# Kernel optimization log

Hardware: AMD Instinct MI355X
Metric: run time of the kernel (lower is better)

## Reference

```python
import jax, jax.numpy as jnp
import numpy as np

B, C, H, W = 4, 512, 32, 32
NUM_HEADS, DIM_HEAD = 16, 32
DIM_ATTN = NUM_HEADS * DIM_HEAD  # 512
N = H * W


def setup_inputs() -> dict:
    key = jax.random.key(0)
    ks = jax.random.split(key, 6)
    s = 0.02
    return {
        "x": jax.random.normal(ks[0], (B, C, H, W), jnp.float32),
        "w_qkv": jax.random.normal(ks[1], (3 * DIM_ATTN, C), jnp.float32) * s,
        "b_qkv": jax.random.normal(ks[2], (3 * DIM_ATTN,), jnp.float32) * s,
        "w_proj": jax.random.normal(ks[3], (C, DIM_ATTN), jnp.float32) * s,
        "b_proj": jax.random.normal(ks[4], (C,), jnp.float32) * s,
        "shared_rel_pos": jax.random.normal(ks[5], (1, NUM_HEADS, N, N), jnp.float32) * s,
    }


def reference(x, w_qkv, b_qkv, w_proj, b_proj, shared_rel_pos):
    b, c, h, w = x.shape
    n = h * w
    scale = DIM_HEAD ** -0.5
    # 1x1 conv == per-pixel matmul over channels
    qkv = jnp.einsum('bchw,oc->bohw', x, w_qkv) + b_qkv[None, :, None, None]
    # [B, heads, 3*dh, N] -> chunk along dim 2 (matches torch .chunk(3, dim=2))
    qkv = qkv.reshape(b, NUM_HEADS, 3 * DIM_HEAD, n)
    q, k, v = jnp.split(qkv, 3, axis=2)          # each [B, heads, dh, N]
    attn = jnp.einsum('bhdi,bhdj->bhij', q, k) * scale  # q^T @ k
    attn = attn + shared_rel_pos
    attn = jax.nn.softmax(attn, axis=-1)
    out = jnp.einsum('bhdj,bhij->bhdi', v, attn)  # v @ attn^T, [B, heads, dh, N]
    out = out.reshape(b, NUM_HEADS * DIM_HEAD, h, w)
    out = jnp.einsum('bchw,oc->bohw', out, w_proj) + b_proj[None, :, None, None]
    return out
```

## Files before the change

kernel.cpp:

```cpp
#include <hip/hip_runtime.h>
#include <cstdint>
#include <cstddef>

#define BATCH 4
#define CIN   512
#define NPIX  1024
#define HEADS 16
#define DH    32
#define DATTN 512
#define O_QKV 1536

typedef unsigned short u16;
typedef __bf16 bf16x4 __attribute__((ext_vector_type(4)));
typedef __bf16 bf16x8 __attribute__((ext_vector_type(8)));
typedef float  f32x4  __attribute__((ext_vector_type(4)));

typedef const __attribute__((address_space(1))) void g1_t;
typedef __attribute__((address_space(3))) void l3_t;

#if defined(__has_builtin)
#if __has_builtin(__builtin_amdgcn_exp2f)
#define EXP2(x) __builtin_amdgcn_exp2f(x)
#endif
#endif
#ifndef EXP2
#define EXP2(x) __expf((x) * 0.6931471805599453f)
#endif

__device__ __forceinline__ u16 f2bf(float f) {
  unsigned u = __float_as_uint(f);
  u += 0x7fffu + ((u >> 16) & 1u);
  return (u16)(u >> 16);
}

__device__ __forceinline__ void gl_lds16(const void* gp, void* lp) {
  __builtin_amdgcn_global_load_lds((g1_t*)gp, (l3_t*)lp, 16, 0, 0);
}

__global__ __launch_bounds__(256) void prep_fused(const float* __restrict__ x,
                                                  const float* __restrict__ w1,
                                                  const float* __restrict__ w2,
                                                  u16* __restrict__ xt,
                                                  u16* __restrict__ o1,
                                                  u16* __restrict__ o2) {
  const int t = threadIdx.x;
  if (blockIdx.x < 512) {
    __shared__ float sT[64][65];
    const int q  = blockIdx.x;
    const int n0 = (q & 15) << 6;
    const int c0 = ((q >> 4) & 7) << 6;
    const int b  = q >> 7;
    const float* xb = x + ((size_t)b * CIN + c0) * NPIX + n0;
#pragma unroll
    for (int i = 0; i < 4; ++i) {
      int r   = i * 16 + (t >> 4);
      int col = (t & 15) << 2;
      float4 v = *reinterpret_cast<const float4*>(&xb[(size_t)r * NPIX + col]);
      sT[r][col + 0] = v.x; sT[r][col + 1] = v.y;
      sT[r][col + 2] = v.z; sT[r][col + 3] = v.w;
    }
    __syncthreads();
#pragma unroll
    for (int i = 0; i < 2; ++i) {
      int nl = t >> 2;
      int ch = (t & 3) + (i << 2);
      u16 tmp[8];
#pragma unroll
      for (int e = 0; e < 8; ++e) tmp[e] = f2bf(sT[(ch << 3) + e][nl]);
      *reinterpret_cast<uint4*>(&xt[((size_t)b * NPIX + n0 + nl) * CIN + c0 + (ch << 3)]) =
          *reinterpret_cast<uint4*>(tmp);
    }
  } else {
    const int idx = (blockIdx.x - 512) * 256 + t;
    const int n1 = (O_QKV * CIN) >> 2;
    float4 v = (idx < n1) ? reinterpret_cast<const float4*>(w1)[idx]
                          : reinterpret_cast<const float4*>(w2)[idx - n1];
    uint2 pk = make_uint2((unsigned)f2bf(v.x) | ((unsigned)f2bf(v.y) << 16),
                          (unsigned)f2bf(v.z) | ((unsigned)f2bf(v.w) << 16));
    if (idx < n1) reinterpret_cast<uint2*>(o1)[idx] = pk;
    else          reinterpret_cast<uint2*>(o2)[idx - n1] = pk;
  }
}

__global__ __launch_bounds__(256) void gemm_qkv_mfma(const u16* __restrict__ wq,
                                                     const u16* __restrict__ xt,
                                                     const float* __restrict__ bias,
                                                     u16* __restrict__ qt,
                                                     u16* __restrict__ kt,
                                                     u16* __restrict__ vt) {
  __shared__ __align__(16) u16 sA[96 * 64];
  __shared__ __align__(16) u16 sB[128 * 64];
  const int t  = threadIdx.x;
  const int w  = t >> 6, l = t & 63, g = l >> 4, ln = l & 15;
  const int n0 = blockIdx.x * 128;
  const int h  = blockIdx.y;
  const int b  = blockIdx.z;
  const int wm = w >> 1, wn = w & 1;

  const u16* wbase = wq + (size_t)h * 96 * CIN;
  const u16* xbase = xt + ((size_t)b * NPIX + n0) * CIN;

  f32x4 acc[3][4];
#pragma unroll
  for (int mi = 0; mi < 3; ++mi)
#pragma unroll
    for (int ni = 0; ni < 4; ++ni) acc[mi][ni] = {0.f, 0.f, 0.f, 0.f};

  for (int k0 = 0; k0 < CIN; k0 += 64) {
#pragma unroll
    for (int i = 0; i < 3; ++i) {
      int chunk = i * 256 + (w << 6) + l;
      gl_lds16(wbase + ((size_t)(chunk >> 3)) * CIN + k0 + ((chunk & 7) << 3),
               (char*)sA + i * 4096 + (w << 10));
    }
#pragma unroll
    for (int i = 0; i < 4; ++i) {
      int chunk = i * 256 + (w << 6) + l;
      gl_lds16(xbase + ((size_t)(chunk >> 3)) * CIN + k0 + ((chunk & 7) << 3),
               (char*)sB + i * 4096 + (w << 10));
    }
    __syncthreads();
#pragma unroll
    for (int kk = 0; kk < 64; kk += 32) {
      bf16x8 af[3], bfr[4];
#pragma unroll
      for (int mi = 0; mi < 3; ++mi)
        af[mi] = *reinterpret_cast<const bf16x8*>(&sA[(48 * wm + 16 * mi + ln) * 64 + kk + (g << 3)]);
#pragma unroll
      for (int ni = 0; ni < 4; ++ni)
        bfr[ni] = *reinterpret_cast<const bf16x8*>(&sB[((wn << 6) + (ni << 4) + ln) * 64 + kk + (g << 3)]);
#pragma unroll
      for (int mi = 0; mi < 3; ++mi)
#pragma unroll
        for (int ni = 0; ni < 4; ++ni)
          acc[mi][ni] = __builtin_amdgcn_mfma_f32_16x16x32_bf16(af[mi], bfr[ni], acc[mi][ni], 0, 0, 0);
    }
    __syncthreads();
  }

  const float QSC = 0.17677669529663687f * 1.4426950408889634f;
  const float* bh = bias + h * 96;
#pragma unroll
  for (int mi = 0; mi < 3; ++mi) {
    const int sec = 48 * wm + 16 * mi;
    const int rb  = sec + (g << 2);
    const float b0 = bh[rb + 0], b1 = bh[rb + 1], b2 = bh[rb + 2], b3 = bh[rb + 3];
#pragma unroll
    for (int ni = 0; ni < 4; ++ni) {
      const int n = n0 + (wn << 6) + (ni << 4) + ln;
      f32x4 a = acc[mi][ni];
      float v0 = a[0] + b0, v1 = a[1] + b1, v2 = a[2] + b2, v3 = a[3] + b3;
      if (sec < 32) { v0 *= QSC; v1 *= QSC; v2 *= QSC; v3 *= QSC; }
      u16 e0 = f2bf(v0), e1 = f2bf(v1), e2 = f2bf(v2), e3 = f2bf(v3);
      if (sec < 32) {
        const int d = sec + (g << 2);
        uint2 pk = make_uint2((unsigned)e0 | ((unsigned)e1 << 16),
                              (unsigned)e2 | ((unsigned)e3 << 16));
        *reinterpret_cast<uint2*>(&qt[(((size_t)(b * HEADS + h)) * NPIX + n) * DH + d]) = pk;
      } else if (sec < 64) {
        const int d = sec - 32 + (g << 2);
        uint2 pk = make_uint2((unsigned)e0 | ((unsigned)e1 << 16),
                              (unsigned)e2 | ((unsigned)e3 << 16));
        *reinterpret_cast<uint2*>(&kt[(((size_t)(b * HEADS + h)) * NPIX + n) * DH + d]) = pk;
      } else {
        const int d = sec - 64 + (g << 2);
        u16* vp = &vt[(((size_t)(b * HEADS + h)) * DH + d) * NPIX + n];
        vp[0] = e0; vp[NPIX] = e1; vp[2 * NPIX] = e2; vp[3 * NPIX] = e3;
      }
    }
  }
}

__global__ __launch_bounds__(256, 2) void attn_mfma(const u16* __restrict__ qt,
                                                    const u16* __restrict__ kt,
                                                    const u16* __restrict__ vt,
                                                    const float* __restrict__ rel,
                                                    u16* __restrict__ aout) {
  __shared__ __align__(16) u16 sK[2][2][2048];
  __shared__ __align__(16) u16 sV[2][2][2048];
  __shared__ __align__(16) u16 sP[4][1024];

  const int t  = threadIdx.x;
  const int w  = t >> 6, l = t & 63, g = l >> 4, ln = l & 15;
  const int bid = blockIdx.x;
  const int xcd = bid & 7, sl = bid >> 3;
  const int bp  = sl & 1;
  const int i0  = ((sl >> 1) & 15) << 6;
  const int h   = (xcd << 1) | (sl >> 5);
  const int iw  = w;

  const size_t bh0 = (size_t)((bp * 2 + 0) * HEADS + h);
  const size_t bh1 = (size_t)((bp * 2 + 1) * HEADS + h);

  const int sc_r  = t >> 3;
  const int sc_kc = (t & 7) ^ (sc_r & 7) ^ ((sc_r >> 3) & 1);
  const int sc_vc = (t & 7) ^ (sc_r & 7);
  const size_t kro = ((size_t)((sc_r << 1) | (sc_kc >> 2))) * DH + ((sc_kc & 3) << 3);
  const u16* ksrc0 = kt + bh0 * NPIX * DH + kro;
  const u16* ksrc1 = kt + bh1 * NPIX * DH + kro;
  const u16* vsrc0 = vt + (bh0 * DH + sc_r) * NPIX + (sc_vc << 3);
  const u16* vsrc1 = vt + (bh1 * DH + sc_r) * NPIX + (sc_vc << 3);
  char* kBase = (char*)&sK[0][0][0] + (w << 10);
  char* vBase = (char*)&sV[0][0][0] + (w << 10);

#define STAGE(s_, p_) do {                                               \
    gl_lds16(ksrc0 + (size_t)(s_) * 2048, kBase + (p_) * 8192);          \
    gl_lds16(ksrc1 + (size_t)(s_) * 2048, kBase + (p_) * 8192 + 4096);   \
    gl_lds16(vsrc0 + (size_t)(s_) * 64,   vBase + (p_) * 8192);          \
    gl_lds16(vsrc1 + (size_t)(s_) * 64,   vBase + (p_) * 8192 + 4096);   \
  } while (0)

  STAGE(0, 0);

  bf16x8 qf0 = *reinterpret_cast<const bf16x8*>(
      qt + (bh0 * NPIX + i0 + (iw << 4) + ln) * DH + (g << 3));
  bf16x8 qf1 = *reinterpret_cast<const bf16x8*>(
      qt + (bh1 * NPIX + i0 + (iw << 4) + ln) * DH + (g << 3));

  const float* relp = rel + ((size_t)h * NPIX + i0 + (iw << 4) + (g << 2)) * NPIX +
                      (ln << 2);
  f32x4 relA4[4], relB4[4];
#pragma unroll
  for (int v = 0; v < 4; ++v)
    relA4[v] = *reinterpret_cast<const f32x4*>(relp + (size_t)v * NPIX);

  f32x4 vzero = {0.f, 0.f, 0.f, 0.f};
  f32x4 accO0[2] = {vzero, vzero};
  f32x4 accO1[2] = {vzero, vzero};
  f32x4 l_lane0 = vzero, l_lane1 = vzero;

  u16* sPw = &sP[w][0];
  const float LOG2E = 1.4426950408889634f;

  for (int s = 0; s < 16; ++s) {
    const int p = s & 1;
    __syncthreads();
    if (s < 15) {
      STAGE(s + 1, p ^ 1);
#pragma unroll
      for (int v = 0; v < 4; ++v)
        relB4[v] = *reinterpret_cast<const f32x4*>(relp + (size_t)v * NPIX + ((s + 1) << 6));
    }

#pragma unroll
    for (int b2 = 0; b2 < 2; ++b2) {
      const u16* Kb = &sK[p][b2][0];
      const u16* Vb = &sV[p][b2][0];
      const bf16x8 qf = b2 ? qf1 : qf0;

      f32x4 sfr[4];
      __builtin_amdgcn_s_setprio(1);
#pragma unroll
      for (int jj = 0; jj < 4; ++jj) {
        const int r  = (ln << 1) + (jj >> 1);
        const int ks = ((((jj & 1) << 2) | g) ^ (r & 7)) ^ ((r >> 3) & 1);
        bf16x8 kf = *reinterpret_cast<const bf16x8*>(Kb + r * 64 + ks * 8);
        sfr[jj] = __builtin_amdgcn_mfma_f32_16x16x32_bf16(qf, kf, vzero, 0, 0, 0);
      }
      __builtin_amdgcn_s_setprio(0);

#pragma unroll
      for (int v = 0; v < 4; ++v) {
        float p0 = EXP2(fmaf(relA4[v][0], LOG2E, sfr[0][v]));
        float p1 = EXP2(fmaf(relA4[v][1], LOG2E, sfr[1][v]));
        float p2 = EXP2(fmaf(relA4[v][2], LOG2E, sfr[2][v]));
        float p3 = EXP2(fmaf(relA4[v][3], LOG2E, sfr[3][v]));
        if (b2) l_lane1[v] += (p0 + p1) + (p2 + p3);
        else    l_lane0[v] += (p0 + p1) + (p2 + p3);
        bf16x4 pk;
        pk[0] = (__bf16)p0; pk[1] = (__bf16)p1; pk[2] = (__bf16)p2; pk[3] = (__bf16)p3;
        const int rw = (g << 2) + v;
        *reinterpret_cast<bf16x4*>(
            sPw + rw * 64 + ((((ln >> 1) ^ (rw & 7)) << 3) | ((ln & 1) << 2))) = pk;
      }

      __builtin_amdgcn_s_setprio(1);
#pragma unroll
      for (int kc = 0; kc < 2; ++kc) {
        const int lc = (kc << 2) | g;
        bf16x8 pa = *reinterpret_cast<const bf16x8*>(sPw + ln * 64 + ((lc ^ (ln & 7)) << 3));
#pragma unroll
        for (int dc = 0; dc < 2; ++dc) {
          const int d  = (dc << 4) + ln;
          const int vs = lc ^ (d & 7);
          bf16x8 vf = *reinterpret_cast<const bf16x8*>(Vb + d * 64 + vs * 8);
          if (b2) accO1[dc] = __builtin_amdgcn_mfma_f32_16x16x32_bf16(pa, vf, accO1[dc], 0, 0, 0);
          else    accO0[dc] = __builtin_amdgcn_mfma_f32_16x16x32_bf16(pa, vf, accO0[dc], 0, 0, 0);
        }
      }
      __builtin_amdgcn_s_setprio(0);
    }

    if (s < 15) {
#pragma unroll
      for (int v = 0; v < 4; ++v) relA4[v] = relB4[v];
    }
  }
#undef STAGE

#pragma unroll
  for (int v = 0; v < 4; ++v) {
    float ls = l_lane0[v];
    ls += __shfl_xor(ls, 1);
    ls += __shfl_xor(ls, 2);
    ls += __shfl_xor(ls, 4);
    ls += __shfl_xor(ls, 8);
    const float inv = 1.f / ls;
    const size_t row = (size_t)(bp * 2 + 0) * NPIX + i0 + (iw << 4) + (g << 2) + v;
    aout[row * DATTN + (h << 5) + ln]      = f2bf(accO0[0][v] * inv);
    aout[row * DATTN + (h << 5) + 16 + ln] = f2bf(accO0[1][v] * inv);
  }
#pragma unroll
  for (int v = 0; v < 4; ++v) {
    float ls = l_lane1[v];
    ls += __shfl_xor(ls, 1);
    ls += __shfl_xor(ls, 2);
    ls += __shfl_xor(ls, 4);
    ls += __shfl_xor(ls, 8);
    const float inv = 1.f / ls;
    const size_t row = (size_t)(bp * 2 + 1) * NPIX + i0 + (iw << 4) + (g << 2) + v;
    aout[row * DATTN + (h << 5) + ln]      = f2bf(accO1[0][v] * inv);
    aout[row * DATTN + (h << 5) + 16 + ln] = f2bf(accO1[1][v] * inv);
  }
}

__global__ __launch_bounds__(256) void gemm_proj_mfma(const u16* __restrict__ wp,
                                                      const u16* __restrict__ at,
                                                      const float* __restrict__ bias,
                                                      float* __restrict__ out) {
  __shared__ __align__(16) u16 sA[64 * 64];
  __shared__ __align__(16) u16 sB[128 * 64];
  const int t  = threadIdx.x;
  const int w  = t >> 6, l = t & 63, g = l >> 4, ln = l & 15;
  const int n0 = blockIdx.x * 128;
  const int o0 = blockIdx.y * 64;
  const int b  = blockIdx.z;
  const int wm = w >> 1, wn = w & 1;

  const u16* wbase = wp + (size_t)o0 * DATTN;
  const u16* abase = at + ((size_t)b * NPIX + n0) * DATTN;

  f32x4 acc[2][4];
#pragma unroll
  for (int mi = 0; mi < 2; ++mi)
#pragma unroll
    for (int ni = 0; ni < 4; ++ni) acc[mi][ni] = {0.f, 0.f, 0.f, 0.f};

  for (int k0 = 0; k0 < DATTN; k0 += 64) {
#pragma unroll
    for (int i = 0; i < 2; ++i) {
      int chunk = i * 256 + (w << 6) + l;
      gl_lds16(wbase + ((size_t)(chunk >> 3)) * DATTN + k0 + ((chunk & 7) << 3),
               (char*)sA + i * 4096 + (w << 10));
    }
#pragma unroll
    for (int i = 0; i < 4; ++i) {
      int chunk = i * 256 + (w << 6) + l;
      gl_lds16(abase + ((size_t)(chunk >> 3)) * DATTN + k0 + ((chunk & 7) << 3),
               (char*)sB + i * 4096 + (w << 10));
    }
    __syncthreads();
#pragma unroll
    for (int kk = 0; kk < 64; kk += 32) {
      bf16x8 af[2], bfr[4];
#pragma unroll
      for (int mi = 0; mi < 2; ++mi)
        af[mi] = *reinterpret_cast<const bf16x8*>(&sA[((wm << 5) + (mi << 4) + ln) * 64 + kk + (g << 3)]);
#pragma unroll
      for (int ni = 0; ni < 4; ++ni)
        bfr[ni] = *reinterpret_cast<const bf16x8*>(&sB[((wn << 6) + (ni << 4) + ln) * 64 + kk + (g << 3)]);
#pragma unroll
      for (int mi = 0; mi < 2; ++mi)
#pragma unroll
        for (int ni = 0; ni < 4; ++ni)
          acc[mi][ni] = __builtin_amdgcn_mfma_f32_16x16x32_bf16(af[mi], bfr[ni], acc[mi][ni], 0, 0, 0);
    }
    __syncthreads();
  }

#pragma unroll
  for (int mi = 0; mi < 2; ++mi) {
    const int o = o0 + (wm << 5) + (mi << 4) + (g << 2);
    const float b0 = bias[o], b1 = bias[o + 1], b2 = bias[o + 2], b3 = bias[o + 3];
#pragma unroll
    for (int ni = 0; ni < 4; ++ni) {
      const int n = n0 + (wn << 6) + (ni << 4) + ln;
      float* op = &out[((size_t)b * DATTN + o) * NPIX + n];
      op[0]        = acc[mi][ni][0] + b0;
      op[NPIX]     = acc[mi][ni][1] + b1;
      op[2 * NPIX] = acc[mi][ni][2] + b2;
      op[3 * NPIX] = acc[mi][ni][3] + b3;
    }
  }
}

extern "C" void kernel_launch(void* const* d_in, const int* in_sizes, int n_in,
                              void* d_out, int out_size, void* d_ws, size_t ws_size,
                              hipStream_t stream) {
  (void)in_sizes; (void)n_in; (void)out_size; (void)ws_size;
  const float* x      = (const float*)d_in[0];
  const float* w_qkv  = (const float*)d_in[1];
  const float* b_qkv  = (const float*)d_in[2];
  const float* w_proj = (const float*)d_in[3];
  const float* b_proj = (const float*)d_in[4];
  const float* rel    = (const float*)d_in[5];
  float* out = (float*)d_out;

  u16* xt    = (u16*)d_ws;
  u16* wq_bf = xt + (size_t)BATCH * NPIX * CIN;
  u16* wp_bf = wq_bf + (size_t)O_QKV * CIN;
  u16* qt    = wp_bf + (size_t)DATTN * DATTN;
  u16* kt    = qt + (size_t)BATCH * HEADS * NPIX * DH;
  u16* vt    = kt + (size_t)BATCH * HEADS * NPIX * DH;
  u16* aout  = vt + (size_t)BATCH * HEADS * NPIX * DH;

  prep_fused<<<1536, 256, 0, stream>>>(x, w_qkv, w_proj, xt, wq_bf, wp_bf);
  gemm_qkv_mfma<<<dim3(NPIX / 128, HEADS, BATCH), 256, 0, stream>>>(wq_bf, xt, b_qkv, qt, kt, vt);
  attn_mfma<<<512, 256, 0, stream>>>(qt, kt, vt, rel, aout);
  gemm_proj_mfma<<<dim3(NPIX / 128, DATTN / 64, BATCH), 256, 0, stream>>>(wp_bf, aout, b_proj, out);
}
```

Before: 62.74 us.

## Split attention key range across two wave groups and merge partial sums

The attention kernel now launches 512 threads per block. The upper four waves process the second half of the key/value sequence, and the lower four process the first half, so each wave runs half as many loop iterations. Partial output accumulators and row sums from the second half are passed through shared memory and added before normalisation. This needs no max rescaling, because the softmax has no max subtraction. The goal is more waves in flight and shorter per-wave latency on the key loop, at the cost of doubled LDS staging, an extra merge step with barriers, and a possible cap on occupancy from the larger shared memory footprint.

```diff
diff --git a/kernel.cpp b/kernel.cpp
--- a/kernel.cpp
+++ b/kernel.cpp
@@ -171,14 +171,14 @@
   }
 }
 
-__global__ __launch_bounds__(256, 2) void attn_mfma(const u16* __restrict__ qt,
+__global__ __launch_bounds__(512, 4) void attn_mfma(const u16* __restrict__ qt,
                                                     const u16* __restrict__ kt,
                                                     const u16* __restrict__ vt,
                                                     const float* __restrict__ rel,
                                                     u16* __restrict__ aout) {
-  __shared__ __align__(16) u16 sK[2][2][2048];
-  __shared__ __align__(16) u16 sV[2][2][2048];
-  __shared__ __align__(16) u16 sP[4][1024];
+  __shared__ __align__(16) u16 sK[2][2][2][2048];
+  __shared__ __align__(16) u16 sV[2][2][2][2048];
+  __shared__ __align__(16) u16 sP[8][1024];
 
   const int t  = threadIdx.x;
   const int w  = t >> 6, l = t & 63, g = l >> 4, ln = l & 15;
@@ -187,27 +187,37 @@
   const int bp  = sl & 1;
   const int i0  = ((sl >> 1) & 15) << 6;
   const int h   = (xcd << 1) | (sl >> 5);
-  const int iw  = w;
+  const int iw  = w & 3;
+  const int jh  = w >> 2;
 
   const size_t bh0 = (size_t)((bp * 2 + 0) * HEADS + h);
   const size_t bh1 = (size_t)((bp * 2 + 1) * HEADS + h);
 
-  const int sc_r  = t >> 3;
-  const int sc_kc = (t & 7) ^ (sc_r & 7) ^ ((sc_r >> 3) & 1);
-  const int sc_vc = (t & 7) ^ (sc_r & 7);
-  const size_t kro = ((size_t)((sc_r << 1) | (sc_kc >> 2))) * DH + ((sc_kc & 3) << 3);
-  const u16* ksrc0 = kt + bh0 * NPIX * DH + kro;
-  const u16* ksrc1 = kt + bh1 * NPIX * DH + kro;
-  const u16* vsrc0 = vt + (bh0 * DH + sc_r) * NPIX + (sc_vc << 3);
-  const u16* vsrc1 = vt + (bh1 * DH + sc_r) * NPIX + (sc_vc << 3);
-  char* kBase = (char*)&sK[0][0][0] + (w << 10);
-  char* vBase = (char*)&sV[0][0][0] + (w << 10);
-
-#define STAGE(s_, p_) do {                                               \
-    gl_lds16(ksrc0 + (size_t)(s_) * 2048, kBase + (p_) * 8192);          \
-    gl_lds16(ksrc1 + (size_t)(s_) * 2048, kBase + (p_) * 8192 + 4096);   \
-    gl_lds16(vsrc0 + (size_t)(s_) * 64,   vBase + (p_) * 8192);          \
-    gl_lds16(vsrc1 + (size_t)(s_) * 64,   vBase + (p_) * 8192 + 4096);   \
+  const int sb2  = iw >> 1;
+  const bool isK = (iw & 1) == 0;
+  const size_t sbh = sb2 ? bh1 : bh0;
+  const u16* src[4];
+#pragma unroll
+  for (int i = 0; i < 4; ++i) {
+    const int c = i * 64 + l;
+    const int r = c >> 3, slot = c & 7;
+    if (isK) {
+      const int kc = slot ^ (r & 7) ^ ((r >> 3) & 1);
+      src[i] = kt + sbh * NPIX * DH +
+               ((size_t)((jh << 9) + ((r << 1) | (kc >> 2)))) * DH + ((kc & 3) << 3);
+    } else {
+      const int vc = slot ^ (r & 7);
+      src[i] = vt + (sbh * DH + r) * NPIX + (jh << 9) + (vc << 3);
+    }
+  }
+  char* dstBase = isK ? (char*)&sK[0][jh][sb2][0] : (char*)&sV[0][jh][sb2][0];
+  const size_t sstep = isK ? 2048 : 64;
+
+#define STAGE(s_, p_) do {                                                   \
+    gl_lds16(src[0] + (size_t)(s_) * sstep, dstBase + (p_) * 16384);         \
+    gl_lds16(src[1] + (size_t)(s_) * sstep, dstBase + (p_) * 16384 + 1024);  \
+    gl_lds16(src[2] + (size_t)(s_) * sstep, dstBase + (p_) * 16384 + 2048);  \
+    gl_lds16(src[3] + (size_t)(s_) * sstep, dstBase + (p_) * 16384 + 3072);  \
   } while (0)
 
   STAGE(0, 0);
@@ -218,7 +228,7 @@
       qt + (bh1 * NPIX + i0 + (iw << 4) + ln) * DH + (g << 3));
 
   const float* relp = rel + ((size_t)h * NPIX + i0 + (iw << 4) + (g << 2)) * NPIX +
-                      (ln << 2);
+                      (jh << 9) + (ln << 2);
   f32x4 relA4[4], relB4[4];
 #pragma unroll
   for (int v = 0; v < 4; ++v)
@@ -232,10 +242,10 @@
   u16* sPw = &sP[w][0];
   const float LOG2E = 1.4426950408889634f;
 
-  for (int s = 0; s < 16; ++s) {
+  for (int s = 0; s < 8; ++s) {
     const int p = s & 1;
     __syncthreads();
-    if (s < 15) {
+    if (s < 7) {
       STAGE(s + 1, p ^ 1);
 #pragma unroll
       for (int v = 0; v < 4; ++v)
@@ -244,8 +254,8 @@
 
 #pragma unroll
     for (int b2 = 0; b2 < 2; ++b2) {
-      const u16* Kb = &sK[p][b2][0];
-      const u16* Vb = &sV[p][b2][0];
+      const u16* Kb = &sK[p][jh][b2][0];
+      const u16* Vb = &sV[p][jh][b2][0];
       const bf16x8 qf = b2 ? qf1 : qf0;
 
       f32x4 sfr[4];
@@ -291,36 +301,57 @@
       __builtin_amdgcn_s_setprio(0);
     }
 
-    if (s < 15) {
+    if (s < 7) {
 #pragma unroll
       for (int v = 0; v < 4; ++v) relA4[v] = relB4[v];
     }
   }
 #undef STAGE
 
-#pragma unroll
-  for (int v = 0; v < 4; ++v) {
-    float ls = l_lane0[v];
-    ls += __shfl_xor(ls, 1);
-    ls += __shfl_xor(ls, 2);
-    ls += __shfl_xor(ls, 4);
-    ls += __shfl_xor(ls, 8);
-    const float inv = 1.f / ls;
-    const size_t row = (size_t)(bp * 2 + 0) * NPIX + i0 + (iw << 4) + (g << 2) + v;
-    aout[row * DATTN + (h << 5) + ln]      = f2bf(accO0[0][v] * inv);
-    aout[row * DATTN + (h << 5) + 16 + ln] = f2bf(accO0[1][v] * inv);
-  }
-#pragma unroll
-  for (int v = 0; v < 4; ++v) {
-    float ls = l_lane1[v];
-    ls += __shfl_xor(ls, 1);
-    ls += __shfl_xor(ls, 2);
-    ls += __shfl_xor(ls, 4);
-    ls += __shfl_xor(ls, 8);
-    const float inv = 1.f / ls;
-    const size_t row = (size_t)(bp * 2 + 1) * NPIX + i0 + (iw << 4) + (g << 2) + v;
-    aout[row * DATTN + (h << 5) + ln]      = f2bf(accO1[0][v] * inv);
-    aout[row * DATTN + (h << 5) + 16 + ln] = f2bf(accO1[1][v] * inv);
+  __syncthreads();
+  float* mrg = (float*)&sK[0][0][0][0];
+  if (jh == 1) {
+    float* mp = mrg + ((size_t)((iw << 6) + l)) * 24;
+    *reinterpret_cast<f32x4*>(mp +  0) = accO0[0];
+    *reinterpret_cast<f32x4*>(mp +  4) = accO0[1];
+    *reinterpret_cast<f32x4*>(mp +  8) = l_lane0;
+    *reinterpret_cast<f32x4*>(mp + 12) = accO1[0];
+    *reinterpret_cast<f32x4*>(mp + 16) = accO1[1];
+    *reinterpret_cast<f32x4*>(mp + 20) = l_lane1;
+  }
+  __syncthreads();
+  if (jh == 0) {
+    const float* mp = mrg + ((size_t)((iw << 6) + l)) * 24;
+    f32x4 o00 = accO0[0] + *reinterpret_cast<const f32x4*>(mp + 0);
+    f32x4 o01 = accO0[1] + *reinterpret_cast<const f32x4*>(mp + 4);
+    f32x4 lv0 = l_lane0 + *reinterpret_cast<const f32x4*>(mp + 8);
+    f32x4 o10 = accO1[0] + *reinterpret_cast<const f32x4*>(mp + 12);
+    f32x4 o11 = accO1[1] + *reinterpret_cast<const f32x4*>(mp + 16);
+    f32x4 lv1 = l_lane1 + *reinterpret_cast<const f32x4*>(mp + 20);
+#pragma unroll
+    for (int v = 0; v < 4; ++v) {
+      float ls = lv0[v];
+      ls += __shfl_xor(ls, 1);
+      ls += __shfl_xor(ls, 2);
+      ls += __shfl_xor(ls, 4);
+      ls += __shfl_xor(ls, 8);
+      const float inv = 1.f / ls;
+      const size_t row = (size_t)(bp * 2 + 0) * NPIX + i0 + (iw << 4) + (g << 2) + v;
+      aout[row * DATTN + (h << 5) + ln]      = f2bf(o00[v] * inv);
+      aout[row * DATTN + (h << 5) + 16 + ln] = f2bf(o01[v] * inv);
+    }
+#pragma unroll
+    for (int v = 0; v < 4; ++v) {
+      float ls = lv1[v];
+      ls += __shfl_xor(ls, 1);
+      ls += __shfl_xor(ls, 2);
+      ls += __shfl_xor(ls, 4);
+      ls += __shfl_xor(ls, 8);
+      const float inv = 1.f / ls;
+      const size_t row = (size_t)(bp * 2 + 1) * NPIX + i0 + (iw << 4) + (g << 2) + v;
+      aout[row * DATTN + (h << 5) + ln]      = f2bf(o10[v] * inv);
+      aout[row * DATTN + (h << 5) + 16 + ln] = f2bf(o11[v] * inv);
+    }
   }
 }
 
@@ -416,6 +447,6 @@
 
   prep_fused<<<1536, 256, 0, stream>>>(x, w_qkv, w_proj, xt, wq_bf, wp_bf);
   gemm_qkv_mfma<<<dim3(NPIX / 128, HEADS, BATCH), 256, 0, stream>>>(wq_bf, xt, b_qkv, qt, kt, vt);
-  attn_mfma<<<512, 256, 0, stream>>>(qt, kt, vt, rel, aout);
+  attn_mfma<<<512, 512, 0, stream>>>(qt, kt, vt, rel, aout);
   gemm_proj_mfma<<<dim3(NPIX / 128, DATTN / 64, BATCH), 256, 0, stream>>>(wp_bf, aout, b_proj, out);
 }
```

New measurement: 58.60 us. 1.07x faster.
